# Kernel tuning notes

Hardware: AMD Instinct MI355X
Metric: run time of the kernel (lower is better)

## Reference

```python
import jax, jax.numpy as jnp
import numpy as np

H_DIM = 2048
N_HEADS = 16

def setup_inputs() -> dict:
    key = jax.random.key(0)
    ks = jax.random.split(key, 9)
    B, T, C = 2, 2048, H_DIM
    scale = 1.0 / np.sqrt(C)  # lecun_normal approx
    src = jax.random.normal(ks[0], (B, T, C), dtype=jnp.float32)
    Wq = jax.random.normal(ks[1], (C, H_DIM), dtype=jnp.float32) * scale
    Wk = jax.random.normal(ks[2], (C, H_DIM), dtype=jnp.float32) * scale
    Wv = jax.random.normal(ks[3], (C, H_DIM), dtype=jnp.float32) * scale
    Wo = jax.random.normal(ks[4], (H_DIM, H_DIM), dtype=jnp.float32) * scale
    bq = jnp.zeros((H_DIM,), jnp.float32)
    bk = jnp.zeros((H_DIM,), jnp.float32)
    bv = jnp.zeros((H_DIM,), jnp.float32)
    bo = jnp.zeros((H_DIM,), jnp.float32)
    return {"src": src, "Wq": Wq, "bq": bq, "Wk": Wk, "bk": bk,
            "Wv": Wv, "bv": bv, "Wo": Wo, "bo": bo}

def reference(src, Wq, bq, Wk, bk, Wv, bv, Wo, bo):
    B, T, C = src.shape
    N = N_HEADS
    D = C // N
    def heads(x):  # [B,T,h_dim] -> [B,N,T,D]
        return x.reshape(B, T, N, D).transpose(0, 2, 1, 3)
    q = heads(src @ Wq + bq)
    k = heads(src @ Wk + bk)
    v = heads(src @ Wv + bv)
    # scaled dot-product with causal mask
    scores = jnp.einsum('bntd,bnsd->bnts', q, k) / jnp.sqrt(jnp.float32(D))
    causal = jnp.tril(jnp.ones((T, T), dtype=bool))
    scores = jnp.where(causal[None, None], scores, -jnp.inf)
    attn = jax.nn.softmax(scores, axis=-1)
    out = jnp.einsum('bnts,bnsd->bntd', attn, v)  # dropout is identity (drop_p=0)
    out = out.transpose(0, 2, 1, 3).reshape(B, T, N * D)
    return out @ Wo + bo
```

## Files before the change

kernel.cpp:

```cpp
#include <hip/hip_runtime.h>
#include <hip/hip_bf16.h>

typedef float f32x4 __attribute__((ext_vector_type(4)));
typedef __bf16 bf16x8v __attribute__((ext_vector_type(8)));
typedef __bf16 bf16x4v __attribute__((ext_vector_type(4)));
typedef unsigned uint2v __attribute__((ext_vector_type(2)));
typedef bf16x8v __attribute__((may_alias)) bf16x8;
typedef bf16x4v __attribute__((may_alias)) bf16x4;
typedef uint2v __attribute__((may_alias)) u32x2;

typedef __attribute__((address_space(1))) const void gvoid_t;
typedef __attribute__((address_space(3))) void lvoid_t;

#define DEVINL __device__ __forceinline__

#define BDIM 2
#define TDIM 2048
#define CDIM 2048
#define NHEAD 16
#define DHEAD 128
#define MROWS 4096
#define WSZ ((size_t)CDIM * CDIM)
#define XSZ ((size_t)MROWS * CDIM)

#define BARRIER_LGKM() asm volatile("s_waitcnt lgkmcnt(0)\ns_barrier" ::: "memory")

DEVINL __bf16 f2bf(float f) {
  unsigned u = __builtin_bit_cast(unsigned, f);
  u += 0x7fffu + ((u >> 16) & 1u);
  unsigned short h = (unsigned short)(u >> 16);
  return __builtin_bit_cast(__bf16, h);
}

DEVINL unsigned pk2bf_trunc(float lo, float hi) {
  return __builtin_amdgcn_perm(__builtin_bit_cast(unsigned, hi),
                               __builtin_bit_cast(unsigned, lo), 0x07060302);
}

DEVINL void gl2lds16(const void* g, void* l) {
  __builtin_amdgcn_global_load_lds((gvoid_t*)g, (lvoid_t*)l, 16, 0, 0);
}

DEVINL int wave_detect(const unsigned* __restrict__ w) {
  const int l = threadIdx.x & 63;
  const unsigned word = w[l];
  const unsigned e = (word >> 7) & 0xFFu;
  const int vote = (e >= 0x70u && e <= 0x87u) ? 1 : 0;
  const unsigned long long m = __ballot(vote);
  return (__popcll(m) >= 32) ? 1 : 0;
}

__global__ __launch_bounds__(256) void prologue(
    const void* __restrict__ src, __bf16* __restrict__ srcbf, int n8,
    const void* __restrict__ b0, const void* __restrict__ b1,
    const void* __restrict__ b2, const void* __restrict__ b3,
    float* __restrict__ biasf, const void* __restrict__ w0,
    const void* __restrict__ w1, const void* __restrict__ w2,
    const void* __restrict__ w3, __bf16* __restrict__ wt,
    int* __restrict__ cnt) {
  __shared__ __attribute__((aligned(16))) __bf16 tile[64][68];
  const int fl = wave_detect((const unsigned*)src);
  const int bi = blockIdx.x;
  if (bi < 4096) {
    const int i = bi * 256 + threadIdx.x;
    if (i >= n8) return;
    if (fl) {
      ((bf16x8*)srcbf)[i] = ((const bf16x8*)src)[i];
    } else {
      const float* f = (const float*)src + (size_t)i * 8;
      bf16x8v v;
#pragma unroll
      for (int j = 0; j < 8; ++j) v[j] = f2bf(f[j]);
      ((bf16x8*)srcbf)[i] = v;
    }
    return;
  }
  if (bi < 4128) {
    if (bi == 4096 && threadIdx.x == 0) *cnt = 0;
    const int i = (bi - 4096) * 256 + threadIdx.x;
    const void* b = (i < 2048) ? b0 : (i < 4096) ? b1 : (i < 6144) ? b2 : b3;
    const int idx = i & 2047;
    biasf[i] = fl ? (float)((const __bf16*)b)[idx] : ((const float*)b)[idx];
    return;
  }
  const int idx = bi - 4128;
  const int z = idx >> 10, rem = idx & 1023;
  const int by = rem >> 5, bx = rem & 31;
  const void* W = (z == 0) ? w0 : (z == 1) ? w1 : (z == 2) ? w2 : w3;
  __bf16* Wt = wt + (size_t)z * WSZ;
  const int tx = threadIdx.x & 63, ty = threadIdx.x >> 6;
  const int k0 = bx * 64, n0 = by * 64;
#pragma unroll
  for (int i = ty; i < 64; i += 4) {
    const size_t off = (size_t)(k0 + i) * CDIM + n0 + tx;
    const float v = fl ? (float)((const __bf16*)W)[off] : ((const float*)W)[off];
    tile[i][tx] = f2bf(v);
  }
  __syncthreads();
#pragma unroll
  for (int i = ty; i < 64; i += 4)
    Wt[(size_t)(n0 + i) * CDIM + k0 + tx] = tile[tx][i];
}

template <int MODE>
__global__ __launch_bounds__(512, 4) void gemmring(
    const __bf16* __restrict__ A, const __bf16* __restrict__ Bt,
    const float* __restrict__ bias, __bf16* __restrict__ qb,
    __bf16* __restrict__ kb, __bf16* __restrict__ vtb,
    const unsigned* __restrict__ srcw, void* __restrict__ outp) {
  constexpr int K = CDIM;
  constexpr int NKT = K / 64;
  __shared__ __attribute__((aligned(16))) __bf16 Asl[3][128 * 32];
  __shared__ __attribute__((aligned(16))) __bf16 Bsl[3][256 * 32];

  const int tid = threadIdx.x;
  const int w = tid >> 6, l = tid & 63;
  const int quad = l >> 4, l16 = l & 15;
  const int wm = w >> 2, wn = w & 3;

  const int bid = blockIdx.x;
  const int bm = bid & 31, bn = bid >> 5;
  const int m0 = bm * 128, n0 = bn * 256;

  const int ls = (tid & 7) ^ ((tid >> 3) & 7);
  const int rbase = 2 * (tid >> 3) + (ls >> 2);
  const int cb8 = (ls & 3) * 8;
  const __bf16* gAh = A + (size_t)(m0 + rbase) * K + cb8;
  const __bf16* gBh = Bt + (size_t)(n0 + rbase) * K + cb8;

  const int L2 = l16 >> 1;
  const int physr = (((l16 & 1) << 2) + quad) ^ L2;
  const int lane_e = L2 * 64 + physr * 8;

  __bf16 *a0 = (__bf16*)Asl[0], *a1 = (__bf16*)Asl[1], *a2 = (__bf16*)Asl[2];
  __bf16 *b0 = (__bf16*)Bsl[0], *b1 = (__bf16*)Bsl[1], *b2 = (__bf16*)Bsl[2];

#define STAGE_A(dst, h)                                                   \
  gl2lds16(gAh + (size_t)(((h) >> 1) * 64 + ((h) & 1) * 32), (dst) + w * 512)
#define STAGE_B(dst, h, e)                                                \
  gl2lds16(gBh + (size_t)(e) * 128 * K +                                  \
               (((h) >> 1) * 64 + ((h) & 1) * 32),                        \
           (dst) + (e) * 4096 + w * 512)

  f32x4 acc[4][4];
#pragma unroll
  for (int i = 0; i < 4; ++i)
#pragma unroll
    for (int j = 0; j < 4; ++j) acc[i][j] = (f32x4){0.f, 0.f, 0.f, 0.f};

  STAGE_A(a0, 0); STAGE_B(b0, 0, 0); STAGE_B(b0, 0, 1);
  STAGE_A(a1, 1); STAGE_B(b1, 1, 0); STAGE_B(b1, 1, 1);
  asm volatile("s_waitcnt vmcnt(3)" ::: "memory");
  __builtin_amdgcn_sched_barrier(0);
  __builtin_amdgcn_s_barrier();

#define MFMA8(NF0)                                                        \
  __builtin_amdgcn_s_setprio(1);                                          \
  _Pragma("unroll") for (int mi = 0; mi < 4; ++mi) {                      \
    acc[mi][(NF0)] = __builtin_amdgcn_mfma_f32_16x16x32_bf16(             \
        afr[mi], bfr[0], acc[mi][(NF0)], 0, 0, 0);                        \
    acc[mi][(NF0) + 1] = __builtin_amdgcn_mfma_f32_16x16x32_bf16(         \
        afr[mi], bfr[1], acc[mi][(NF0) + 1], 0, 0, 0);                    \
  }                                                                       \
  __builtin_amdgcn_s_setprio(0);

#define LGKM_BAR()                                                        \
  __builtin_amdgcn_s_barrier();                                           \
  asm volatile("s_waitcnt lgkmcnt(0)" ::: "memory");                      \
  __builtin_amdgcn_sched_barrier(0)

  for (int kt = 0; kt < NKT; ++kt) {
    const int h0 = 2 * kt;
    const bool st = (kt < NKT - 1);
    bf16x8 afr[4], bfr[2];

#pragma unroll
    for (int mi = 0; mi < 4; ++mi)
      afr[mi] = *(const bf16x8*)&a0[(wm * 64 + mi * 16) * 32 + lane_e];
    bfr[0] = *(const bf16x8*)&b0[(wn * 64 + 0 * 16) * 32 + lane_e];
    bfr[1] = *(const bf16x8*)&b0[(wn * 64 + 1 * 16) * 32 + lane_e];
    if (st) { STAGE_A(a2, h0 + 2); STAGE_B(b2, h0 + 2, 0); }
    LGKM_BAR();
    MFMA8(0)
    __builtin_amdgcn_s_barrier();

    bfr[0] = *(const bf16x8*)&b0[(wn * 64 + 2 * 16) * 32 + lane_e];
    bfr[1] = *(const bf16x8*)&b0[(wn * 64 + 3 * 16) * 32 + lane_e];
    if (st) { STAGE_B(b2, h0 + 2, 1); }
    LGKM_BAR();
    MFMA8(2)
    if (st)
      asm volatile("s_waitcnt vmcnt(3)" ::: "memory");
    else
      asm volatile("s_waitcnt vmcnt(0)" ::: "memory");
    __builtin_amdgcn_sched_barrier(0);
    __builtin_amdgcn_s_barrier();

#pragma unroll
    for (int mi = 0; mi < 4; ++mi)
      afr[mi] = *(const bf16x8*)&a1[(wm * 64 + mi * 16) * 32 + lane_e];
    bfr[0] = *(const bf16x8*)&b1[(wn * 64 + 0 * 16) * 32 + lane_e];
    bfr[1] = *(const bf16x8*)&b1[(wn * 64 + 1 * 16) * 32 + lane_e];
    if (st) { STAGE_A(a0, h0 + 3); STAGE_B(b0, h0 + 3, 0); }
    LGKM_BAR();
    MFMA8(0)
    __builtin_amdgcn_s_barrier();

    bfr[0] = *(const bf16x8*)&b1[(wn * 64 + 2 * 16) * 32 + lane_e];
    bfr[1] = *(const bf16x8*)&b1[(wn * 64 + 3 * 16) * 32 + lane_e];
    if (st) { STAGE_B(b0, h0 + 3, 1); }
    LGKM_BAR();
    MFMA8(2)
    asm volatile("s_waitcnt vmcnt(3)" ::: "memory");
    __builtin_amdgcn_sched_barrier(0);
    __builtin_amdgcn_s_barrier();

    __bf16* t;
    t = a0; a0 = a2; a2 = a1; a1 = t;
    t = b0; b0 = b2; b2 = b1; b1 = t;
  }
#undef MFMA8
#undef LGKM_BAR
#undef STAGE_A
#undef STAGE_B

  if (MODE == 0) {
    const int mat = n0 >> 11;
#pragma unroll
    for (int nf = 0; nf < 4; ++nf) {
      const int n = n0 + wn * 64 + nf * 16 + l16;
      const int nn = n & 2047;
      const int h = nn >> 7, d = nn & 127;
      const float bv = bias[n];
#pragma unroll
      for (int mi = 0; mi < 4; ++mi) {
        const int mbase = m0 + wm * 64 + mi * 16 + quad * 4;
        const int bb = mbase >> 11, t = mbase & 2047;
        if (mat == 2) {
          bf16x4v v4;
#pragma unroll
          for (int r = 0; r < 4; ++r) v4[r] = f2bf(acc[mi][nf][r] + bv);
          *(bf16x4*)&vtb[((size_t)(bb * NHEAD + h) * DHEAD + d) * TDIM + t] = v4;
        } else {
          __bf16* op = (mat == 0) ? qb : kb;
#pragma unroll
          for (int r = 0; r < 4; ++r)
            op[((size_t)(bb * NHEAD + h) * TDIM + t + r) * DHEAD + d] =
                f2bf(acc[mi][nf][r] + bv);
        }
      }
    }
  } else {
    const int ofl = wave_detect(srcw);
#pragma unroll
    for (int nf = 0; nf < 4; ++nf) {
      const int n = n0 + wn * 64 + nf * 16 + l16;
      const float bv = bias[n];
#pragma unroll
      for (int mi = 0; mi < 4; ++mi) {
#pragma unroll
        for (int r = 0; r < 4; ++r) {
          const int m = m0 + wm * 64 + mi * 16 + quad * 4 + r;
          const float v = acc[mi][nf][r] + bv;
          if (ofl) ((__bf16*)outp)[(size_t)m * CDIM + n] = f2bf(v);
          else     ((float*)outp)[(size_t)m * CDIM + n] = v;
        }
      }
    }
  }
}

__global__ __launch_bounds__(256, 2) void attn(
    const __bf16* __restrict__ Q, const __bf16* __restrict__ K,
    const __bf16* __restrict__ Vt, __bf16* __restrict__ ctx,
    int* __restrict__ cnt) {
  constexpr float CSC = 0.12753139726f;
  __shared__ __attribute__((aligned(16))) __bf16 Kls[64 * 128];
  __shared__ __attribute__((aligned(16))) __bf16 Vls[128 * 64];
  __shared__ __attribute__((aligned(16))) __bf16 Pls[4][32 * 64];
  __shared__ int jobLds;

  const int tid = threadIdx.x;
  const int w = tid >> 6, l = tid & 63, quad = l >> 4, l16 = l & 15;

  const int krow = tid >> 4;
  const int kcol = tid & 15;
  const int kldsoff = ((kcol ^ krow) * 8);
  const int vrow = tid >> 3;
  const int vcol = tid & 7;
  const int vldsoff = ((vcol ^ (vrow & 7)) * 8);

  for (;;) {
    __syncthreads();
    if (tid == 0) jobLds = atomicAdd(cnt, 1);
    __syncthreads();
    const int j = jobLds;
    if (j >= 512) break;
    const int qt = 15 - (j >> 5);
    const int bh = j & 31;
    const int t0w = qt * 128 + w * 32;
    const __bf16* Qbh = Q + (size_t)bh * TDIM * DHEAD;
    const __bf16* Kbh = K + (size_t)bh * TDIM * DHEAD;
    const __bf16* Vbh = Vt + (size_t)bh * TDIM * DHEAD;

    bf16x8 qf[2][4];
#pragma unroll
    for (int tt = 0; tt < 2; ++tt)
#pragma unroll
      for (int ks = 0; ks < 4; ++ks)
        qf[tt][ks] = *(const bf16x8*)(Qbh +
                     (size_t)(t0w + tt * 16 + l16) * DHEAD + ks * 32 + quad * 8);

    f32x4 oacc[8][2];
#pragma unroll
    for (int dt = 0; dt < 8; ++dt)
#pragma unroll
      for (int tt = 0; tt < 2; ++tt) oacc[dt][tt] = (f32x4){0.f, 0.f, 0.f, 0.f};
    float mrow[2] = {-1e30f, -1e30f};
    float lrow[2] = {0.f, 0.f};

    const int nsb = 2 * (qt + 1);

    bf16x8 kr[4], vr[4];
#pragma unroll
    for (int p = 0; p < 4; ++p)
      kr[p] = *(const bf16x8*)(Kbh + (size_t)(p * 16 + krow) * DHEAD + kcol * 8);
#pragma unroll
    for (int p = 0; p < 4; ++p)
      vr[p] = *(const bf16x8*)(Vbh + (size_t)(p * 32 + vrow) * TDIM + vcol * 8);

    for (int sb = 0; sb < nsb; ++sb) {
      const int s0 = sb * 64;
      BARRIER_LGKM();
#pragma unroll
      for (int p = 0; p < 4; ++p)
        *(bf16x8*)&Kls[(p * 16 + krow) * 128 + kldsoff] = kr[p];
#pragma unroll
      for (int p = 0; p < 4; ++p)
        *(bf16x8*)&Vls[(p * 32 + vrow) * 64 + vldsoff] = vr[p];
      if (sb + 1 < nsb) {
        const int s1 = s0 + 64;
#pragma unroll
        for (int p = 0; p < 4; ++p)
          kr[p] = *(const bf16x8*)(Kbh + (size_t)(s1 + p * 16 + krow) * DHEAD +
                                   kcol * 8);
#pragma unroll
        for (int p = 0; p < 4; ++p)
          vr[p] = *(const bf16x8*)(Vbh + (size_t)(p * 32 + vrow) * TDIM + s1 +
                                   vcol * 8);
      }
      BARRIER_LGKM();
      if (s0 > t0w + 31) continue;

      f32x4 sacc[4][2];
#pragma unroll
      for (int st = 0; st < 4; ++st)
#pragma unroll
        for (int tt = 0; tt < 2; ++tt) sacc[st][tt] = (f32x4){0.f, 0.f, 0.f, 0.f};
      __builtin_amdgcn_s_setprio(1);
#pragma unroll
      for (int ks = 0; ks < 4; ++ks) {
        bf16x8 kf[4];
#pragma unroll
        for (int st = 0; st < 4; ++st)
          kf[st] = *(const bf16x8*)&Kls[(st * 16 + l16) * 128 +
                                        (((ks * 4 + quad) ^ l16) * 8)];
#pragma unroll
        for (int st = 0; st < 4; ++st)
#pragma unroll
          for (int tt = 0; tt < 2; ++tt)
            sacc[st][tt] = __builtin_amdgcn_mfma_f32_16x16x32_bf16(
                kf[st], qf[tt][ks], sacc[st][tt], 0, 0, 0);
      }
      __builtin_amdgcn_s_setprio(0);
      if (s0 + 63 > t0w) {
#pragma unroll
        for (int st = 0; st < 4; ++st)
#pragma unroll
          for (int tt = 0; tt < 2; ++tt)
#pragma unroll
            for (int r = 0; r < 4; ++r) {
              const int s = s0 + st * 16 + quad * 4 + r;
              const int t = t0w + tt * 16 + l16;
              if (s > t) sacc[st][tt][r] = -1e30f;
            }
      }
#pragma unroll
      for (int tt = 0; tt < 2; ++tt) {
        float vm = -1e30f;
#pragma unroll
        for (int st = 0; st < 4; ++st)
#pragma unroll
          for (int r = 0; r < 4; ++r) vm = fmaxf(vm, sacc[st][tt][r]);
        vm = fmaxf(vm, __shfl_xor(vm, 16));
        vm = fmaxf(vm, __shfl_xor(vm, 32));
        if (__ballot((vm - mrow[tt]) * CSC > 8.0f)) {
          const float mn = fmaxf(mrow[tt], vm);
          const float alpha = exp2f((mrow[tt] - mn) * CSC);
          lrow[tt] *= alpha;
#pragma unroll
          for (int dt = 0; dt < 8; ++dt)
#pragma unroll
            for (int r = 0; r < 4; ++r) oacc[dt][tt][r] *= alpha;
          mrow[tt] = mn;
        }
        const float mcur = mrow[tt];
        float rs = 0.f;
#pragma unroll
        for (int st = 0; st < 4; ++st) {
          const float p0 = exp2f((sacc[st][tt][0] - mcur) * CSC);
          const float p1 = exp2f((sacc[st][tt][1] - mcur) * CSC);
          const float p2 = exp2f((sacc[st][tt][2] - mcur) * CSC);
          const float p3 = exp2f((sacc[st][tt][3] - mcur) * CSC);
          rs += (p0 + p1) + (p2 + p3);
          u32x2 pk = {pk2bf_trunc(p0, p1), pk2bf_trunc(p2, p3)};
          *(u32x2*)&Pls[w][(tt * 16 + l16) * 64 +
                           (((st * 2 + (quad >> 1)) ^ (l16 & 7)) * 8) +
                           (quad & 1) * 4] = pk;
        }
        rs += __shfl_xor(rs, 16);
        rs += __shfl_xor(rs, 32);
        lrow[tt] += rs;
      }
      asm volatile("s_waitcnt lgkmcnt(0)" ::: "memory");
      __builtin_amdgcn_s_setprio(1);
#pragma unroll
      for (int ks = 0; ks < 2; ++ks) {
        bf16x8 pf[2];
#pragma unroll
        for (int tt = 0; tt < 2; ++tt)
          pf[tt] = *(const bf16x8*)&Pls[w][(tt * 16 + l16) * 64 +
                                           (((ks * 4 + quad) ^ (l16 & 7)) * 8)];
#pragma unroll
        for (int dt = 0; dt < 8; ++dt) {
          const bf16x8 vf =
              *(const bf16x8*)&Vls[(dt * 16 + l16) * 64 +
                                   (((ks * 4 + quad) ^ (l16 & 7)) * 8)];
#pragma unroll
          for (int tt = 0; tt < 2; ++tt)
            oacc[dt][tt] = __builtin_amdgcn_mfma_f32_16x16x32_bf16(
                vf, pf[tt], oacc[dt][tt], 0, 0, 0);
        }
      }
      __builtin_amdgcn_s_setprio(0);
    }

    const int b = bh >> 4, h = bh & 15;
#pragma unroll
    for (int tt = 0; tt < 2; ++tt) {
      const float rinv = 1.0f / lrow[tt];
      const int t = t0w + tt * 16 + l16;
      __bf16* cp = ctx + ((size_t)(b * TDIM + t)) * CDIM + h * DHEAD;
#pragma unroll
      for (int dt = 0; dt < 8; ++dt) {
        bf16x4v v4;
#pragma unroll
        for (int r = 0; r < 4; ++r) v4[r] = f2bf(oacc[dt][tt][r] * rinv);
        *(bf16x4*)&cp[dt * 16 + quad * 4] = v4;
      }
    }
  }
}

extern "C" void kernel_launch(void* const* d_in, const int* in_sizes, int n_in,
                              void* d_out, int out_size, void* d_ws,
                              size_t ws_size, hipStream_t stream) {
  const void* src = d_in[0];
  const void* Wq = d_in[1];
  const void* bq = d_in[2];
  const void* Wk = d_in[3];
  const void* bk = d_in[4];
  const void* Wv = d_in[5];
  const void* bv = d_in[6];
  const void* Wo = d_in[7];
  const void* bo = d_in[8];

  char* wsb = (char*)d_ws;
  int* cnt = (int*)(wsb + 128);
  __bf16* srcbf = (__bf16*)(wsb + 256);
  __bf16* wqt = srcbf + XSZ;
  __bf16* wot = wqt + 3 * WSZ;
  __bf16* qb = wot + WSZ;
  __bf16* kb = qb + XSZ;
  __bf16* vtb = kb + XSZ;
  float* biasf = (float*)(vtb + XSZ);
  __bf16* ctx = srcbf;

  prologue<<<8224, 256, 0, stream>>>(src, srcbf, (int)(XSZ / 8), bq, bk, bv,
                                     bo, biasf, Wq, Wk, Wv, Wo, wqt, cnt);
  gemmring<0><<<768, 512, 0, stream>>>(srcbf, wqt, biasf, qb, kb, vtb,
                                       nullptr, nullptr);
  attn<<<512, 256, 0, stream>>>(qb, kb, vtb, ctx, cnt);
  gemmring<1><<<256, 512, 0, stream>>>(ctx, wot, biasf + 6144, nullptr,
                                       nullptr, nullptr, (const unsigned*)src,
                                       d_out);
}
```

Before: 397.0 us.

## Switch GEMM LDS ring from triple to double buffering for higher occupancy

Cuts the GEMM shared-memory staging from three buffers to two. Each half-step now prefetches only the next sub-tile and waits for all outstanding loads (vmcnt(0)) before the barrier. Launch bounds rise from 4 to 6 blocks per CU so the smaller LDS footprint can hold more resident blocks. The cost is a shallower prefetch distance, which exposes more global-load latency per step, and the higher occupancy target may force register spilling with a 4x4 accumulator array.

Result: slower. 1.488 ms (+274.9%).

```diff
diff --git a/kernel.cpp b/kernel.cpp
--- a/kernel.cpp
+++ b/kernel.cpp
@@ -103,15 +103,15 @@
 }
 
 template <int MODE>
-__global__ __launch_bounds__(512, 4) void gemmring(
+__global__ __launch_bounds__(512, 6) void gemmring(
     const __bf16* __restrict__ A, const __bf16* __restrict__ Bt,
     const float* __restrict__ bias, __bf16* __restrict__ qb,
     __bf16* __restrict__ kb, __bf16* __restrict__ vtb,
     const unsigned* __restrict__ srcw, void* __restrict__ outp) {
   constexpr int K = CDIM;
   constexpr int NKT = K / 64;
-  __shared__ __attribute__((aligned(16))) __bf16 Asl[3][128 * 32];
-  __shared__ __attribute__((aligned(16))) __bf16 Bsl[3][256 * 32];
+  __shared__ __attribute__((aligned(16))) __bf16 Asl[2][128 * 32];
+  __shared__ __attribute__((aligned(16))) __bf16 Bsl[2][256 * 32];
 
   const int tid = threadIdx.x;
   const int w = tid >> 6, l = tid & 63;
@@ -132,8 +132,10 @@
   const int physr = (((l16 & 1) << 2) + quad) ^ L2;
   const int lane_e = L2 * 64 + physr * 8;
 
-  __bf16 *a0 = (__bf16*)Asl[0], *a1 = (__bf16*)Asl[1], *a2 = (__bf16*)Asl[2];
-  __bf16 *b0 = (__bf16*)Bsl[0], *b1 = (__bf16*)Bsl[1], *b2 = (__bf16*)Bsl[2];
+  __bf16* a0 = (__bf16*)Asl[0];
+  __bf16* a1 = (__bf16*)Asl[1];
+  __bf16* b0 = (__bf16*)Bsl[0];
+  __bf16* b1 = (__bf16*)Bsl[1];
 
 #define STAGE_A(dst, h)                                                   \
   gl2lds16(gAh + (size_t)(((h) >> 1) * 64 + ((h) & 1) * 32), (dst) + w * 512)
@@ -149,8 +151,7 @@
     for (int j = 0; j < 4; ++j) acc[i][j] = (f32x4){0.f, 0.f, 0.f, 0.f};
 
   STAGE_A(a0, 0); STAGE_B(b0, 0, 0); STAGE_B(b0, 0, 1);
-  STAGE_A(a1, 1); STAGE_B(b1, 1, 0); STAGE_B(b1, 1, 1);
-  asm volatile("s_waitcnt vmcnt(3)" ::: "memory");
+  asm volatile("s_waitcnt vmcnt(0)" ::: "memory");
   __builtin_amdgcn_sched_barrier(0);
   __builtin_amdgcn_s_barrier();
 
@@ -169,6 +170,11 @@
   asm volatile("s_waitcnt lgkmcnt(0)" ::: "memory");                      \
   __builtin_amdgcn_sched_barrier(0)
 
+#define VM0_BAR()                                                         \
+  asm volatile("s_waitcnt vmcnt(0)" ::: "memory");                        \
+  __builtin_amdgcn_sched_barrier(0);                                      \
+  __builtin_amdgcn_s_barrier()
+
   for (int kt = 0; kt < NKT; ++kt) {
     const int h0 = 2 * kt;
     const bool st = (kt < NKT - 1);
@@ -179,48 +185,36 @@
       afr[mi] = *(const bf16x8*)&a0[(wm * 64 + mi * 16) * 32 + lane_e];
     bfr[0] = *(const bf16x8*)&b0[(wn * 64 + 0 * 16) * 32 + lane_e];
     bfr[1] = *(const bf16x8*)&b0[(wn * 64 + 1 * 16) * 32 + lane_e];
-    if (st) { STAGE_A(a2, h0 + 2); STAGE_B(b2, h0 + 2, 0); }
+    STAGE_A(a1, h0 + 1); STAGE_B(b1, h0 + 1, 0); STAGE_B(b1, h0 + 1, 1);
     LGKM_BAR();
     MFMA8(0)
     __builtin_amdgcn_s_barrier();
 
     bfr[0] = *(const bf16x8*)&b0[(wn * 64 + 2 * 16) * 32 + lane_e];
     bfr[1] = *(const bf16x8*)&b0[(wn * 64 + 3 * 16) * 32 + lane_e];
-    if (st) { STAGE_B(b2, h0 + 2, 1); }
     LGKM_BAR();
     MFMA8(2)
-    if (st)
-      asm volatile("s_waitcnt vmcnt(3)" ::: "memory");
-    else
-      asm volatile("s_waitcnt vmcnt(0)" ::: "memory");
-    __builtin_amdgcn_sched_barrier(0);
-    __builtin_amdgcn_s_barrier();
+    VM0_BAR();
 
 #pragma unroll
     for (int mi = 0; mi < 4; ++mi)
       afr[mi] = *(const bf16x8*)&a1[(wm * 64 + mi * 16) * 32 + lane_e];
     bfr[0] = *(const bf16x8*)&b1[(wn * 64 + 0 * 16) * 32 + lane_e];
     bfr[1] = *(const bf16x8*)&b1[(wn * 64 + 1 * 16) * 32 + lane_e];
-    if (st) { STAGE_A(a0, h0 + 3); STAGE_B(b0, h0 + 3, 0); }
+    if (st) { STAGE_A(a0, h0 + 2); STAGE_B(b0, h0 + 2, 0); STAGE_B(b0, h0 + 2, 1); }
     LGKM_BAR();
     MFMA8(0)
     __builtin_amdgcn_s_barrier();
 
     bfr[0] = *(const bf16x8*)&b1[(wn * 64 + 2 * 16) * 32 + lane_e];
     bfr[1] = *(const bf16x8*)&b1[(wn * 64 + 3 * 16) * 32 + lane_e];
-    if (st) { STAGE_B(b0, h0 + 3, 1); }
     LGKM_BAR();
     MFMA8(2)
-    asm volatile("s_waitcnt vmcnt(3)" ::: "memory");
-    __builtin_amdgcn_sched_barrier(0);
-    __builtin_amdgcn_s_barrier();
-
-    __bf16* t;
-    t = a0; a0 = a2; a2 = a1; a1 = t;
-    t = b0; b0 = b2; b2 = b1; b1 = t;
+    VM0_BAR();
   }
 #undef MFMA8
 #undef LGKM_BAR
+#undef VM0_BAR
 #undef STAGE_A
 #undef STAGE_B
 
```
